# Kernel optimization log

Measured on AMD Instinct MI355X. Metric: run time of the kernel, lower is better.

## Reference

```python
import jax, jax.numpy as jnp
import numpy as np

NUM_ENT = 50000
NUM_REL = 64
NUM_TRI = 400000
DIN = 128
DOUT = 128
DREL = 128
NUM_HEAD = 8
DH = DOUT // NUM_HEAD


def setup_inputs() -> dict:
    key = jax.random.key(0)
    ks = jax.random.split(key, 9)
    emb_ent = jax.random.normal(ks[0], (NUM_ENT, DIN), jnp.float32)
    emb_rel = jax.random.normal(ks[1], (NUM_REL, DREL), jnp.float32)
    heads = jax.random.randint(ks[2], (NUM_TRI,), 0, NUM_ENT)
    rels = jax.random.randint(ks[3], (NUM_TRI,), 0, NUM_REL)
    tails = jax.random.randint(ks[4], (NUM_TRI,), 0, NUM_ENT)
    triplets = jnp.stack([heads, rels, tails], axis=-1)
    # xavier-normal-like init (stored as [in, out]; torch Linear applies x @ W.T)
    Wa = jax.random.normal(ks[5], (2 * DIN + DREL, DOUT), jnp.float32) * (2.0 / (2 * DIN + DREL + DOUT)) ** 0.5
    ba = jnp.zeros((DOUT,), jnp.float32)
    attn_vec = jax.random.normal(ks[6], (1, NUM_HEAD, DH), jnp.float32) * 0.1
    Wg = jax.random.normal(ks[7], (DIN + DREL, DOUT), jnp.float32) * (2.0 / (DIN + DREL + DOUT)) ** 0.5
    bg = jnp.zeros((DOUT,), jnp.float32)
    return {"emb_ent": emb_ent, "emb_rel": emb_rel, "triplets": triplets,
            "Wa": Wa, "ba": ba, "attn_vec": attn_vec, "Wg": Wg, "bg": bg}


def reference(emb_ent, emb_rel, triplets, Wa, ba, attn_vec, Wg, bg):
    num_ent = emb_ent.shape[0]
    n_head, d_hid = attn_vec.shape[1], attn_vec.shape[2]
    head, rel, tail = triplets[:, 0], triplets[:, 1], triplets[:, 2]

    # in-degree of each entity (as attention-softmax denominator for self_rel)
    ent_freq = jax.ops.segment_sum(jnp.ones(tail.shape, jnp.float32), tail,
                                   num_segments=num_ent)[:, None]
    # torch adds 1e-16 to all entries iff any entry is zero
    ent_freq = ent_freq + jnp.where(jnp.any(ent_freq == 0.0), 1e-16, 0.0)

    # mean relation embedding of incoming edges per entity -> self-loop relation
    self_rel = jax.ops.segment_sum(emb_rel[rel], tail, num_segments=num_ent) / ent_freq

    # append self-loops: one per entity
    emb_rels = jnp.concatenate([emb_rel[rel], self_rel], axis=0)       # [E+N, dr]
    ar = jnp.arange(num_ent)
    head_all = jnp.concatenate([head, ar], axis=0)                     # [E+N]
    tail_all = jnp.concatenate([tail, ar], axis=0)                     # [E+N]

    # attention logits per edge per head
    feat_att = jnp.concatenate([emb_ent[tail_all], emb_ent[head_all], emb_rels], axis=-1)
    h = jnp.tanh(feat_att @ Wa + ba).reshape(-1, n_head, d_hid)
    attn_raw = jnp.sum(h * attn_vec, axis=-1, keepdims=True)           # [E+N, H, 1]

    # segment softmax over edges sharing a tail (every segment has a self-loop)
    amax = jax.ops.segment_max(attn_raw, tail_all, num_segments=num_ent)
    attn_val = jnp.exp(attn_raw - amax[tail_all])
    asum = jax.ops.segment_sum(attn_val, tail_all, num_segments=num_ent)
    beta = attn_val / (asum[tail_all] + 1e-16)                         # [E+N, H, 1]

    # message projection and weighted aggregation
    msg = (jnp.concatenate([emb_ent[head_all], emb_rels], axis=-1) @ Wg + bg)
    msg = msg.reshape(-1, n_head, d_hid)
    out = jax.ops.segment_sum(beta * msg, tail_all, num_segments=num_ent)
    return out.reshape(num_ent, -1)
```

## Files before the change

kernel.cpp:

```cpp
#include <hip/hip_runtime.h>
#include <math.h>

#define NUM_ENT  50000
#define NUM_REL  64
#define NUM_TRI  400000
#define DIN      128
#define CAP      64

#define PACK_BLOCKS  24
#define SMALL_BLOCKS 64
#define ZERO_BLOCKS  196
#define PREP_BLOCKS  (PACK_BLOCKS + SMALL_BLOCKS + ZERO_BLOCKS)

#define ENT_BLOCKS   782
#define SCAT_BLOCKS  391

typedef __attribute__((ext_vector_type(8))) short bf16x8;
typedef __attribute__((ext_vector_type(8))) unsigned short u16x8;
typedef __attribute__((ext_vector_type(4))) float f32x4;

__device__ __forceinline__ float4 f4add(float4 a, float4 b) {
    return make_float4(a.x + b.x, a.y + b.y, a.z + b.z, a.w + b.w);
}

__device__ __forceinline__ unsigned short f2bf(float f) {
    unsigned u = __float_as_uint(f);
    unsigned r = ((u >> 16) & 1u) + 0x7fffu;
    return (unsigned short)((u + r) >> 16);
}
__device__ __forceinline__ float bf2f(unsigned short h) {
    return __uint_as_float(((unsigned)h) << 16);
}
__device__ __forceinline__ float4 ldbf4(const unsigned short* p) {
    ushort4 u = *(const ushort4*)p;
    return make_float4(bf2f(u.x), bf2f(u.y), bf2f(u.z), bf2f(u.w));
}
__device__ __forceinline__ void ldbf8(const unsigned short* p, float4* lo, float4* hi) {
    u16x8 u = *(const u16x8*)p;
    *lo = make_float4(bf2f(u[0]), bf2f(u[1]), bf2f(u[2]), bf2f(u[3]));
    *hi = make_float4(bf2f(u[4]), bf2f(u[5]), bf2f(u[6]), bf2f(u[7]));
}

__device__ __forceinline__ float tanhf_fast(float x) {
    float e = __expf(2.f * x);
    return 1.f - 2.f * __builtin_amdgcn_rcpf(e + 1.f);
}
__device__ __forceinline__ float tanh_dot4(float4 x, float4 av) {
    return tanhf_fast(x.x) * av.x + tanhf_fast(x.y) * av.y +
           tanhf_fast(x.z) * av.z + tanhf_fast(x.w) * av.w;
}

__global__ __launch_bounds__(256) void k_prep(const float* __restrict__ emb_rel,
                                              const float* __restrict__ Wa,
                                              const float* __restrict__ Wg,
                                              unsigned short* __restrict__ Bpack,
                                              unsigned short* __restrict__ TaTg,
                                              int* __restrict__ deg) {
    __shared__ float s[DIN];
    int b = blockIdx.x;
    int tid = threadIdx.x;

    if (b < PACK_BLOCKS) {
        for (int i = 0; i < 8; i++) {
            int idx = b * 2048 + i * 256 + tid;
            int j    = idx & 7;
            int lane = (idx >> 3) & 63;
            int ks   = (idx >> 9) & 3;
            int t    = (idx >> 11) & 7;
            int w    = idx >> 14;
            int k = ks * 32 + ((lane >> 4) << 3) + j;
            int n = t * 16 + (lane & 15);
            const float* W = (w == 0) ? Wa : (w == 1) ? (Wa + 128 * DIN) : Wg;
            Bpack[idx] = f2bf(W[k * DIN + n]);
        }
    } else if (b < PACK_BLOCKS + SMALL_BLOCKS) {
        int row = b - PACK_BLOCKS;
        if (tid < DIN) s[tid] = emb_rel[row * DIN + tid];
        __syncthreads();
        int j = tid & 127;
        const float* W = (tid < 128) ? (Wa + 256 * DIN) : (Wg + 128 * DIN);
        float acc = 0.f;
#pragma unroll 8
        for (int k = 0; k < DIN; k++) acc += s[k] * W[k * DIN + j];
        int pos = row * 256 + 8 * (j >> 2) + (j & 3) + ((tid < 128) ? 0 : 4);
        TaTg[pos] = f2bf(acc);
    } else {
        int idx = (b - PACK_BLOCKS - SMALL_BLOCKS) * 256 + tid;
        if (idx < NUM_ENT) deg[idx] = 0;
    }
}

__global__ __launch_bounds__(256) void k_scat(const int* __restrict__ trip,
                                              int* __restrict__ deg,
                                              int* __restrict__ elist) {
    int b = blockIdx.x;
    int tid = threadIdx.x;
    int i0 = b * 1024 + tid * 4;
    if (i0 < NUM_TRI) {
        const int4* tp = (const int4*)&trip[i0 * 3];
        int4 A = tp[0], B4 = tp[1], C4 = tp[2];
        int hs[4] = {A.x, A.w, B4.z, C4.y};
        int rs[4] = {A.y, B4.x, B4.w, C4.z};
        int ts[4] = {A.z, B4.y, C4.x, C4.w};
#pragma unroll
        for (int u = 0; u < 4; u++) {
            int pos = atomicAdd(&deg[ts[u]], 1);
            if (pos < CAP) elist[ts[u] * CAP + pos] = (hs[u] << 6) | rs[u];
        }
    }
}

__global__ __launch_bounds__(256) void k_gemm(const float* __restrict__ X,
                                              const unsigned short* __restrict__ Bpack,
                                              const float* __restrict__ ba,
                                              const float* __restrict__ bg,
                                              unsigned short* __restrict__ Pt,
                                              unsigned short* __restrict__ PhGh) {
    __shared__ unsigned short As[64][136];
    int b = blockIdx.x;
    int tid = threadIdx.x;

    int m0 = b * 64;
    for (int i = 0; i < 8; i++) {
        int v = tid + i * 256;
        int row = v >> 5;
        int c4 = v & 31;
        int gr = m0 + row;
        if (gr >= NUM_ENT) gr = NUM_ENT - 1;
        float4 x = *(const float4*)&X[gr * DIN + c4 * 4];
        ushort4 h;
        h.x = f2bf(x.x); h.y = f2bf(x.y); h.z = f2bf(x.z); h.w = f2bf(x.w);
        *(ushort4*)&As[row][c4 * 4] = h;
    }
    __syncthreads();

    int w = tid >> 6;
    int q = tid & 63;
    int quad = q >> 4;
    int lrow = w * 16 + (q & 15);
    int gr = m0 + lrow;

    bf16x8 a[4];
#pragma unroll
    for (int ks = 0; ks < 4; ks++)
        a[ks] = *(const bf16x8*)&As[lrow][ks * 32 + quad * 8];

    const bf16x8* Bp = (const bf16x8*)Bpack;
#pragma unroll
    for (int s = 0; s < 3; s++) {
        f32x4 acc[8];
#pragma unroll
        for (int t = 0; t < 8; t++) acc[t] = (f32x4){0.f, 0.f, 0.f, 0.f};
#pragma unroll
        for (int ks = 0; ks < 4; ks++) {
#pragma unroll
            for (int t = 0; t < 8; t++) {
                bf16x8 wf = Bp[((s * 8 + t) * 4 + ks) * 64 + q];
                acc[t] = __builtin_amdgcn_mfma_f32_16x16x32_bf16(wf, a[ks], acc[t], 0, 0, 0);
            }
        }
        if (gr < NUM_ENT) {
#pragma unroll
            for (int t = 0; t < 8; t++) {
                int n0 = t * 16 + quad * 4;
                float4 bb = make_float4(0.f, 0.f, 0.f, 0.f);
                if (s == 0) bb = *(const float4*)&ba[n0];
                if (s == 2) bb = *(const float4*)&bg[n0];
                ushort4 o;
                o.x = f2bf(acc[t][0] + bb.x);
                o.y = f2bf(acc[t][1] + bb.y);
                o.z = f2bf(acc[t][2] + bb.z);
                o.w = f2bf(acc[t][3] + bb.w);
                if (s == 0) {
                    *(ushort4*)&Pt[gr * DIN + n0] = o;
                } else {
                    *(ushort4*)&PhGh[gr * 256 + 2 * n0 + ((s == 1) ? 0 : 4)] = o;
                }
            }
        }
    }
}

__global__ __launch_bounds__(256) void k_fused(const int* __restrict__ elist,
                                               const int* __restrict__ deg_arr,
                                               const unsigned short* __restrict__ Pt,
                                               const unsigned short* __restrict__ PhGh,
                                               const unsigned short* __restrict__ TaTg,
                                               const float* __restrict__ attn_vec,
                                               float* __restrict__ out) {
    int tid = threadIdx.x;
    int wv = tid >> 6;
    int lane = tid & 63;
    int half = lane >> 5;
    int q = lane & 31;
    int t = blockIdx.x * 4 + wv;
    int deg = deg_arr[t];
    if (deg > CAP) deg = CAP;
    int c = q * 4;

    float4 pt4 = ldbf4(&Pt[t * DIN + c]);
    float4 av4 = *(const float4*)&attn_vec[c];

    int eall = elist[t * CAP + lane];

    float l = 0.f;
    float4 acc = make_float4(0.f, 0.f, 0.f, 0.f);
    float4 sTa = make_float4(0.f, 0.f, 0.f, 0.f);
    float4 sTg = make_float4(0.f, 0.f, 0.f, 0.f);

    int it = half;
    for (; it + 2 < deg; it += 4) {
        int e0 = __shfl(eall, it);
        int e1 = __shfl(eall, it + 2);
        int h0 = e0 >> 6, r0 = e0 & 63;
        int h1 = e1 >> 6, r1 = e1 & 63;
        float4 ta0, tg0, ph0, gh0, ta1, tg1, ph1, gh1;
        ldbf8(&TaTg[r0 * 256 + q * 8], &ta0, &tg0);
        ldbf8(&PhGh[h0 * 256 + q * 8], &ph0, &gh0);
        ldbf8(&TaTg[r1 * 256 + q * 8], &ta1, &tg1);
        ldbf8(&PhGh[h1 * 256 + q * 8], &ph1, &gh1);

        sTa = f4add(sTa, f4add(ta0, ta1));
        sTg = f4add(sTg, f4add(tg0, tg1));
        float4 pa0 = f4add(ph0, ta0);
        float4 gm0 = f4add(gh0, tg0);
        float4 pa1 = f4add(ph1, ta1);
        float4 gm1 = f4add(gh1, tg1);
        float p0 = tanh_dot4(f4add(pt4, pa0), av4);
        float p1 = tanh_dot4(f4add(pt4, pa1), av4);
        p0 += __shfl_xor(p0, 1);
        p0 += __shfl_xor(p0, 2);
        p1 += __shfl_xor(p1, 1);
        p1 += __shfl_xor(p1, 2);
        float w0 = __expf(p0);
        float w1 = __expf(p1);
        l += w0 + w1;
        acc.x += w0 * gm0.x + w1 * gm1.x;
        acc.y += w0 * gm0.y + w1 * gm1.y;
        acc.z += w0 * gm0.z + w1 * gm1.z;
        acc.w += w0 * gm0.w + w1 * gm1.w;
    }
    {
        int e = __shfl(eall, it & (CAP - 1));
        if (it < deg) {
            int h = e >> 6;
            int r = e & 63;
            float4 ta, tg, ph, gh;
            ldbf8(&TaTg[r * 256 + q * 8], &ta, &tg);
            ldbf8(&PhGh[h * 256 + q * 8], &ph, &gh);
            sTa = f4add(sTa, ta);
            sTg = f4add(sTg, tg);
            float4 pa = f4add(ph, ta);
            float4 gm = f4add(gh, tg);
            float p = tanh_dot4(f4add(pt4, pa), av4);
            p += __shfl_xor(p, 1);
            p += __shfl_xor(p, 2);
            float w = __expf(p);
            l += w;
            acc.x += w * gm.x; acc.y += w * gm.y; acc.z += w * gm.z; acc.w += w * gm.w;
        }
    }

    l     += __shfl_xor(l, 32);
    acc.x += __shfl_xor(acc.x, 32);
    acc.y += __shfl_xor(acc.y, 32);
    acc.z += __shfl_xor(acc.z, 32);
    acc.w += __shfl_xor(acc.w, 32);
    sTa.x += __shfl_xor(sTa.x, 32);
    sTa.y += __shfl_xor(sTa.y, 32);
    sTa.z += __shfl_xor(sTa.z, 32);
    sTa.w += __shfl_xor(sTa.w, 32);
    sTg.x += __shfl_xor(sTg.x, 32);
    sTg.y += __shfl_xor(sTg.y, 32);
    sTg.z += __shfl_xor(sTg.z, 32);
    sTg.w += __shfl_xor(sTg.w, 32);

    {
        float inv = (deg > 0) ? __builtin_amdgcn_rcpf((float)deg) : 0.f;
        float4 pa, gm;
        ldbf8(&PhGh[t * 256 + q * 8], &pa, &gm);
        pa.x += sTa.x * inv; pa.y += sTa.y * inv; pa.z += sTa.z * inv; pa.w += sTa.w * inv;
        gm.x += sTg.x * inv; gm.y += sTg.y * inv; gm.z += sTg.z * inv; gm.w += sTg.w * inv;
        float p = tanh_dot4(f4add(pt4, pa), av4);
        p += __shfl_xor(p, 1);
        p += __shfl_xor(p, 2);
        float w = __expf(p);
        l += w;
        acc.x += w * gm.x; acc.y += w * gm.y; acc.z += w * gm.z; acc.w += w * gm.w;
    }
    float invl = 1.f / (l + 1e-16f);
    if (half == 0) {
        *(float4*)&out[t * DIN + c] =
            make_float4(acc.x * invl, acc.y * invl, acc.z * invl, acc.w * invl);
    }
}

extern "C" void kernel_launch(void* const* d_in, const int* in_sizes, int n_in,
                              void* d_out, int out_size, void* d_ws, size_t ws_size,
                              hipStream_t stream) {
    const float* emb_ent  = (const float*)d_in[0];
    const float* emb_rel  = (const float*)d_in[1];
    const int*   trip     = (const int*)d_in[2];
    const float* Wa       = (const float*)d_in[3];
    const float* ba       = (const float*)d_in[4];
    const float* attn_vec = (const float*)d_in[5];
    const float* Wg       = (const float*)d_in[6];
    const float* bg       = (const float*)d_in[7];
    float* out = (float*)d_out;

    unsigned short* wsh = (unsigned short*)d_ws;
    unsigned short* Pt    = wsh;
    unsigned short* PhGh  = wsh + 6400000;
    unsigned short* TaTg  = wsh + 19200000;
    unsigned short* Bpack = wsh + 19216384;
    int* deg   = (int*)(wsh + 19265536);
    int* elist = deg + 50000;

    k_prep<<<PREP_BLOCKS, 256, 0, stream>>>(emb_rel, Wa, Wg, Bpack, TaTg, deg);

    k_scat<<<SCAT_BLOCKS, 256, 0, stream>>>(trip, deg, elist);

    k_gemm<<<ENT_BLOCKS, 256, 0, stream>>>(emb_ent, Bpack, ba, bg, Pt, PhGh);

    k_fused<<<NUM_ENT / 4, 256, 0, stream>>>(elist, deg,
                                             Pt, PhGh, TaTg, attn_vec, out);
}
```

Before: 185.5 us.

## Merge scatter and GEMM kernels, pad degree counters, simplify tanh-dot math

```diff
diff --git a/kernel.cpp b/kernel.cpp
--- a/kernel.cpp
+++ b/kernel.cpp
@@ -7,13 +7,15 @@
 #define DIN      128
 #define CAP      64
 
+#define DEGS     16
+
 #define PACK_BLOCKS  24
 #define SMALL_BLOCKS 64
-#define ZERO_BLOCKS  196
-#define PREP_BLOCKS  (PACK_BLOCKS + SMALL_BLOCKS + ZERO_BLOCKS)
+#define PREP_BLOCKS  (PACK_BLOCKS + SMALL_BLOCKS)
 
 #define ENT_BLOCKS   782
 #define SCAT_BLOCKS  391
+#define MID_BLOCKS   (ENT_BLOCKS + SCAT_BLOCKS)
 
 typedef __attribute__((ext_vector_type(8))) short bf16x8;
 typedef __attribute__((ext_vector_type(8))) unsigned short u16x8;
@@ -41,21 +43,19 @@
     *hi = make_float4(bf2f(u[4]), bf2f(u[5]), bf2f(u[6]), bf2f(u[7]));
 }
 
-__device__ __forceinline__ float tanhf_fast(float x) {
-    float e = __expf(2.f * x);
-    return 1.f - 2.f * __builtin_amdgcn_rcpf(e + 1.f);
-}
-__device__ __forceinline__ float tanh_dot4(float4 x, float4 av) {
-    return tanhf_fast(x.x) * av.x + tanhf_fast(x.y) * av.y +
-           tanhf_fast(x.z) * av.z + tanhf_fast(x.w) * av.w;
+__device__ __forceinline__ float att_p(float4 x, float4 m2av, float sumAv) {
+    float r0 = __builtin_amdgcn_rcpf(__expf(2.f * x.x) + 1.f);
+    float r1 = __builtin_amdgcn_rcpf(__expf(2.f * x.y) + 1.f);
+    float r2 = __builtin_amdgcn_rcpf(__expf(2.f * x.z) + 1.f);
+    float r3 = __builtin_amdgcn_rcpf(__expf(2.f * x.w) + 1.f);
+    return fmaf(m2av.x, r0, fmaf(m2av.y, r1, fmaf(m2av.z, r2, fmaf(m2av.w, r3, sumAv))));
 }
 
 __global__ __launch_bounds__(256) void k_prep(const float* __restrict__ emb_rel,
                                               const float* __restrict__ Wa,
                                               const float* __restrict__ Wg,
                                               unsigned short* __restrict__ Bpack,
-                                              unsigned short* __restrict__ TaTg,
-                                              int* __restrict__ deg) {
+                                              unsigned short* __restrict__ TaTg) {
     __shared__ float s[DIN];
     int b = blockIdx.x;
     int tid = threadIdx.x;
@@ -73,7 +73,7 @@
             const float* W = (w == 0) ? Wa : (w == 1) ? (Wa + 128 * DIN) : Wg;
             Bpack[idx] = f2bf(W[k * DIN + n]);
         }
-    } else if (b < PACK_BLOCKS + SMALL_BLOCKS) {
+    } else {
         int row = b - PACK_BLOCKS;
         if (tid < DIN) s[tid] = emb_rel[row * DIN + tid];
         __syncthreads();
@@ -84,98 +84,94 @@
         for (int k = 0; k < DIN; k++) acc += s[k] * W[k * DIN + j];
         int pos = row * 256 + 8 * (j >> 2) + (j & 3) + ((tid < 128) ? 0 : 4);
         TaTg[pos] = f2bf(acc);
-    } else {
-        int idx = (b - PACK_BLOCKS - SMALL_BLOCKS) * 256 + tid;
-        if (idx < NUM_ENT) deg[idx] = 0;
-    }
-}
-
-__global__ __launch_bounds__(256) void k_scat(const int* __restrict__ trip,
-                                              int* __restrict__ deg,
-                                              int* __restrict__ elist) {
-    int b = blockIdx.x;
-    int tid = threadIdx.x;
-    int i0 = b * 1024 + tid * 4;
-    if (i0 < NUM_TRI) {
-        const int4* tp = (const int4*)&trip[i0 * 3];
-        int4 A = tp[0], B4 = tp[1], C4 = tp[2];
-        int hs[4] = {A.x, A.w, B4.z, C4.y};
-        int rs[4] = {A.y, B4.x, B4.w, C4.z};
-        int ts[4] = {A.z, B4.y, C4.x, C4.w};
-#pragma unroll
-        for (int u = 0; u < 4; u++) {
-            int pos = atomicAdd(&deg[ts[u]], 1);
-            if (pos < CAP) elist[ts[u] * CAP + pos] = (hs[u] << 6) | rs[u];
-        }
-    }
-}
-
-__global__ __launch_bounds__(256) void k_gemm(const float* __restrict__ X,
-                                              const unsigned short* __restrict__ Bpack,
-                                              const float* __restrict__ ba,
-                                              const float* __restrict__ bg,
-                                              unsigned short* __restrict__ Pt,
-                                              unsigned short* __restrict__ PhGh) {
+    }
+}
+
+__global__ __launch_bounds__(256) void k_mid(const float* __restrict__ X,
+                                             const unsigned short* __restrict__ Bpack,
+                                             const int* __restrict__ trip,
+                                             const float* __restrict__ ba,
+                                             const float* __restrict__ bg,
+                                             unsigned short* __restrict__ Pt,
+                                             unsigned short* __restrict__ PhGh,
+                                             int* __restrict__ deg,
+                                             int* __restrict__ elist) {
     __shared__ unsigned short As[64][136];
     int b = blockIdx.x;
     int tid = threadIdx.x;
 
-    int m0 = b * 64;
-    for (int i = 0; i < 8; i++) {
-        int v = tid + i * 256;
-        int row = v >> 5;
-        int c4 = v & 31;
-        int gr = m0 + row;
-        if (gr >= NUM_ENT) gr = NUM_ENT - 1;
-        float4 x = *(const float4*)&X[gr * DIN + c4 * 4];
-        ushort4 h;
-        h.x = f2bf(x.x); h.y = f2bf(x.y); h.z = f2bf(x.z); h.w = f2bf(x.w);
-        *(ushort4*)&As[row][c4 * 4] = h;
-    }
-    __syncthreads();
-
-    int w = tid >> 6;
-    int q = tid & 63;
-    int quad = q >> 4;
-    int lrow = w * 16 + (q & 15);
-    int gr = m0 + lrow;
-
-    bf16x8 a[4];
-#pragma unroll
-    for (int ks = 0; ks < 4; ks++)
-        a[ks] = *(const bf16x8*)&As[lrow][ks * 32 + quad * 8];
-
-    const bf16x8* Bp = (const bf16x8*)Bpack;
-#pragma unroll
-    for (int s = 0; s < 3; s++) {
-        f32x4 acc[8];
-#pragma unroll
-        for (int t = 0; t < 8; t++) acc[t] = (f32x4){0.f, 0.f, 0.f, 0.f};
-#pragma unroll
-        for (int ks = 0; ks < 4; ks++) {
-#pragma unroll
-            for (int t = 0; t < 8; t++) {
-                bf16x8 wf = Bp[((s * 8 + t) * 4 + ks) * 64 + q];
-                acc[t] = __builtin_amdgcn_mfma_f32_16x16x32_bf16(wf, a[ks], acc[t], 0, 0, 0);
+    if (b < ENT_BLOCKS) {
+        int m0 = b * 64;
+        for (int i = 0; i < 8; i++) {
+            int v = tid + i * 256;
+            int row = v >> 5;
+            int c4 = v & 31;
+            int gr = m0 + row;
+            if (gr >= NUM_ENT) gr = NUM_ENT - 1;
+            float4 x = *(const float4*)&X[gr * DIN + c4 * 4];
+            ushort4 h;
+            h.x = f2bf(x.x); h.y = f2bf(x.y); h.z = f2bf(x.z); h.w = f2bf(x.w);
+            *(ushort4*)&As[row][c4 * 4] = h;
+        }
+        __syncthreads();
+
+        int w = tid >> 6;
+        int q = tid & 63;
+        int quad = q >> 4;
+        int lrow = w * 16 + (q & 15);
+        int gr = m0 + lrow;
+
+        bf16x8 a[4];
+#pragma unroll
+        for (int ks = 0; ks < 4; ks++)
+            a[ks] = *(const bf16x8*)&As[lrow][ks * 32 + quad * 8];
+
+        const bf16x8* Bp = (const bf16x8*)Bpack;
+#pragma unroll
+        for (int s = 0; s < 3; s++) {
+            f32x4 acc[8];
+#pragma unroll
+            for (int t = 0; t < 8; t++) acc[t] = (f32x4){0.f, 0.f, 0.f, 0.f};
+#pragma unroll
+            for (int ks = 0; ks < 4; ks++) {
+#pragma unroll
+                for (int t = 0; t < 8; t++) {
+                    bf16x8 wf = Bp[((s * 8 + t) * 4 + ks) * 64 + q];
+                    acc[t] = __builtin_amdgcn_mfma_f32_16x16x32_bf16(wf, a[ks], acc[t], 0, 0, 0);
+                }
             }
-        }
-        if (gr < NUM_ENT) {
-#pragma unroll
-            for (int t = 0; t < 8; t++) {
-                int n0 = t * 16 + quad * 4;
-                float4 bb = make_float4(0.f, 0.f, 0.f, 0.f);
-                if (s == 0) bb = *(const float4*)&ba[n0];
-                if (s == 2) bb = *(const float4*)&bg[n0];
-                ushort4 o;
-                o.x = f2bf(acc[t][0] + bb.x);
-                o.y = f2bf(acc[t][1] + bb.y);
-                o.z = f2bf(acc[t][2] + bb.z);
-                o.w = f2bf(acc[t][3] + bb.w);
-                if (s == 0) {
-                    *(ushort4*)&Pt[gr * DIN + n0] = o;
-                } else {
-                    *(ushort4*)&PhGh[gr * 256 + 2 * n0 + ((s == 1) ? 0 : 4)] = o;
+            if (gr < NUM_ENT) {
+#pragma unroll
+                for (int t = 0; t < 8; t++) {
+                    int n0 = t * 16 + quad * 4;
+                    float4 bb = make_float4(0.f, 0.f, 0.f, 0.f);
+                    if (s == 0) bb = *(const float4*)&ba[n0];
+                    if (s == 2) bb = *(const float4*)&bg[n0];
+                    ushort4 o;
+                    o.x = f2bf(acc[t][0] + bb.x);
+                    o.y = f2bf(acc[t][1] + bb.y);
+                    o.z = f2bf(acc[t][2] + bb.z);
+                    o.w = f2bf(acc[t][3] + bb.w);
+                    if (s == 0) {
+                        *(ushort4*)&Pt[gr * DIN + n0] = o;
+                    } else {
+                        *(ushort4*)&PhGh[gr * 256 + 2 * n0 + ((s == 1) ? 0 : 4)] = o;
+                    }
                 }
+            }
+        }
+    } else {
+        int i0 = (b - ENT_BLOCKS) * 1024 + tid * 4;
+        if (i0 < NUM_TRI) {
+            const int4* tp = (const int4*)&trip[i0 * 3];
+            int4 A = tp[0], B4 = tp[1], C4 = tp[2];
+            int hs[4] = {A.x, A.w, B4.z, C4.y};
+            int rs[4] = {A.y, B4.x, B4.w, C4.z};
+            int ts[4] = {A.z, B4.y, C4.x, C4.w};
+#pragma unroll
+            for (int u = 0; u < 4; u++) {
+                int pos = atomicAdd(&deg[ts[u] * DEGS], 1);
+                if (pos < CAP) elist[ts[u] * CAP + pos] = (hs[u] << 6) | rs[u];
             }
         }
     }
@@ -194,12 +190,14 @@
     int half = lane >> 5;
     int q = lane & 31;
     int t = blockIdx.x * 4 + wv;
-    int deg = deg_arr[t];
+    int deg = deg_arr[t * DEGS];
     if (deg > CAP) deg = CAP;
     int c = q * 4;
 
     float4 pt4 = ldbf4(&Pt[t * DIN + c]);
     float4 av4 = *(const float4*)&attn_vec[c];
+    float sumAv = av4.x + av4.y + av4.z + av4.w;
+    float4 m2av = make_float4(-2.f * av4.x, -2.f * av4.y, -2.f * av4.z, -2.f * av4.w);
 
     int eall = elist[t * CAP + lane];
 
@@ -226,8 +224,8 @@
         float4 gm0 = f4add(gh0, tg0);
         float4 pa1 = f4add(ph1, ta1);
         float4 gm1 = f4add(gh1, tg1);
-        float p0 = tanh_dot4(f4add(pt4, pa0), av4);
-        float p1 = tanh_dot4(f4add(pt4, pa1), av4);
+        float p0 = att_p(f4add(pt4, pa0), m2av, sumAv);
+        float p1 = att_p(f4add(pt4, pa1), m2av, sumAv);
         p0 += __shfl_xor(p0, 1);
         p0 += __shfl_xor(p0, 2);
         p1 += __shfl_xor(p1, 1);
@@ -252,7 +250,7 @@
             sTg = f4add(sTg, tg);
             float4 pa = f4add(ph, ta);
             float4 gm = f4add(gh, tg);
-            float p = tanh_dot4(f4add(pt4, pa), av4);
+            float p = att_p(f4add(pt4, pa), m2av, sumAv);
             p += __shfl_xor(p, 1);
             p += __shfl_xor(p, 2);
             float w = __expf(p);
@@ -281,7 +279,7 @@
         ldbf8(&PhGh[t * 256 + q * 8], &pa, &gm);
         pa.x += sTa.x * inv; pa.y += sTa.y * inv; pa.z += sTa.z * inv; pa.w += sTa.w * inv;
         gm.x += sTg.x * inv; gm.y += sTg.y * inv; gm.z += sTg.z * inv; gm.w += sTg.w * inv;
-        float p = tanh_dot4(f4add(pt4, pa), av4);
+        float p = att_p(f4add(pt4, pa), m2av, sumAv);
         p += __shfl_xor(p, 1);
         p += __shfl_xor(p, 2);
         float w = __expf(p);
@@ -314,13 +312,14 @@
     unsigned short* TaTg  = wsh + 19200000;
     unsigned short* Bpack = wsh + 19216384;
     int* deg   = (int*)(wsh + 19265536);
-    int* elist = deg + 50000;
-
-    k_prep<<<PREP_BLOCKS, 256, 0, stream>>>(emb_rel, Wa, Wg, Bpack, TaTg, deg);
-
-    k_scat<<<SCAT_BLOCKS, 256, 0, stream>>>(trip, deg, elist);
-
-    k_gemm<<<ENT_BLOCKS, 256, 0, stream>>>(emb_ent, Bpack, ba, bg, Pt, PhGh);
+    int* elist = deg + 50000 * DEGS;
+
+    hipMemsetAsync(deg, 0, NUM_ENT * DEGS * sizeof(int), stream);
+
+    k_prep<<<PREP_BLOCKS, 256, 0, stream>>>(emb_rel, Wa, Wg, Bpack, TaTg);
+
+    k_mid<<<MID_BLOCKS, 256, 0, stream>>>(emb_ent, Bpack, trip, ba, bg,
+                                          Pt, PhGh, deg, elist);
 
     k_fused<<<NUM_ENT / 4, 256, 0, stream>>>(elist, deg,
                                              Pt, PhGh, TaTg, attn_vec, out);
```

After: 184.3 us. No clear change (-0.7%).
